# Performance work log

Measured on AMD Instinct MI355X. Metric: run time of the kernel, lower is better.

## Reference

```python
import jax, jax.numpy as jnp
import numpy as np

N, D, M, L, DEPTH, WIDTH, MPTS = 2048, 64, 2048, 16, 3, 128, 64
WIN = 2 * L + 1  # 33


def setup_inputs() -> dict:
    key = jax.random.key(0)
    ks = jax.random.split(key, 6)
    # xavier-normal-ish scales to keep sigmoids in a reasonable range
    s0 = float(np.sqrt(2.0 / (D + WIDTH)))
    s1 = float(np.sqrt(2.0 / (2 * WIDTH)))
    s2 = float(np.sqrt(2.0 / (WIDTH + WIN)))
    return {
        "u": jax.random.normal(ks[0], (MPTS, D), dtype=jnp.float32),
        "weight0": jax.random.normal(ks[1], (WIN, WIDTH, D), dtype=jnp.float32) * s0,
        "bias0": jnp.zeros((WIN, WIDTH, 1), dtype=jnp.float32),
        "weight": jax.random.normal(ks[2], (DEPTH - 1, WIN, WIDTH, WIDTH), dtype=jnp.float32) * s1,
        "bias": jnp.zeros((DEPTH - 1, WIN, WIDTH, 1), dtype=jnp.float32),
        "weight_final": jax.random.normal(ks[3], (M, WIN, WIDTH), dtype=jnp.float32) * s2,
        "bias_final": jnp.zeros((M, WIN, 1), dtype=jnp.float32),
        "xi": jax.random.normal(ks[4], (M, N + 2 * L), dtype=jnp.float32) * 0.1,
    }


def reference(u, weight0, bias0, weight, bias, weight_final, bias_final, xi):
    sig = jax.nn.sigmoid
    # first_step: shared per-frequency MLP stack
    u1 = sig(jnp.einsum('jkl,ml->jkm', weight0, u) + bias0)
    for i in range(weight.shape[0]):  # depth-1 hidden layers (small fixed count)
        u1 = sig(jnp.einsum('jkl,jlm->jkm', weight[i], u1) + bias[i])
    G = sig(jnp.einsum('ijk,jkm->ijm', weight_final, u1) + bias_final)
    # sliding-window weighted sum over spectral coeffs, vectorized as a 1D
    # cross-correlation: out[n, p] = sum_{m,j} xi[m, n+j] * G[m, j, p]
    kernel = jnp.transpose(G, (2, 0, 1))
    out = jax.lax.conv_general_dilated(
        xi[None],  # [1, M, N+2L]
        kernel,
        window_strides=(1,),
        padding='VALID',
        dimension_numbers=('NCH', 'OIH', 'NCH'),
    )  # [1, MPTS, N]
    return out[0].T  # [N, MPTS] == torch.cat over iter_prod
```

## Files before the change

kernel.cpp:

```cpp
#include <hip/hip_runtime.h>

#define WIN 33
#define WIDTH 128
#define MPTS 64
#define NN 2048
#define MM 2048
#define DD 64
#define NQ 2080

typedef __bf16 bf16x8 __attribute__((ext_vector_type(8)));
typedef float f32x4 __attribute__((ext_vector_type(4)));

__device__ __forceinline__ unsigned short f2bf(float x) {
  union { float f; unsigned int u; } v; v.f = x;
  unsigned int r = v.u + 0x7FFFu + ((v.u >> 16) & 1u);
  return (unsigned short)(r >> 16);
}
__device__ __forceinline__ float sigf(float x) { return 1.0f / (1.0f + __expf(-x)); }

__device__ __forceinline__ void gll16(const unsigned short* g, unsigned short* l) {
  __builtin_amdgcn_global_load_lds(
      (const __attribute__((address_space(1))) unsigned int*)g,
      (__attribute__((address_space(3))) unsigned int*)l, 16, 0, 0);
}

__global__ __launch_bounds__(256) void k_transpose(const float* __restrict__ xi,
                                                   unsigned short* __restrict__ xiT) {
  __shared__ float ts[64 * 37];
  int qb = blockIdx.x * 32;
  int mb = blockIdx.y * 64;
#pragma unroll
  for (int c = threadIdx.x; c < 512; c += 256) {
    int row = c >> 3, c8 = c & 7;
    float4 v = *(const float4*)&xi[(size_t)(mb + row) * NQ + qb + (c8 << 2)];
    ts[row * 37 + (c8 << 2) + 0] = v.x;
    ts[row * 37 + (c8 << 2) + 1] = v.y;
    ts[row * 37 + (c8 << 2) + 2] = v.z;
    ts[row * 37 + (c8 << 2) + 3] = v.w;
  }
  __syncthreads();
#pragma unroll
  for (int c = threadIdx.x; c < 512; c += 256) {
    int r = c >> 4, mq = c & 15;
    ushort4 h;
    h.x = f2bf(ts[(mq * 4 + 0) * 37 + r]);
    h.y = f2bf(ts[(mq * 4 + 1) * 37 + r]);
    h.z = f2bf(ts[(mq * 4 + 2) * 37 + r]);
    h.w = f2bf(ts[(mq * 4 + 3) * 37 + r]);
    *(ushort4*)&xiT[((size_t)blockIdx.y * NQ + (qb + r)) * 64 + (mq << 2)] = h;
  }
}

__global__ __launch_bounds__(256) void k_mlp(const float* __restrict__ u,
                                             const float* __restrict__ w0,
                                             const float* __restrict__ b0,
                                             const float* __restrict__ w,
                                             const float* __restrict__ bias,
                                             unsigned short* __restrict__ u1bf) {
  constexpr int WS = 72;
  constexpr int AS = 136;
  __shared__ unsigned short ws[128 * WS];
  __shared__ unsigned short actA[64 * AS];
  __shared__ unsigned short actB[64 * AS];
  __shared__ float biass[128];
  int j = blockIdx.x;
  int tid = threadIdx.x;
  int wv = tid >> 6, lane = tid & 63, l15 = lane & 15, l4 = lane >> 4;

#pragma unroll
  for (int c = tid; c < 1024; c += 256) {
    int p = c >> 4, d4 = (c & 15) << 2;
    float4 v = *(const float4*)&u[(size_t)p * DD + d4];
    ushort4 h; h.x = f2bf(v.x); h.y = f2bf(v.y); h.z = f2bf(v.z); h.w = f2bf(v.w);
    *(ushort4*)&actA[p * AS + d4] = h;
  }
#pragma unroll
  for (int c = tid; c < 2048; c += 256) {
    int k = c >> 4, d4 = (c & 15) << 2;
    float4 v = *(const float4*)&w0[((size_t)j * 128 + k) * DD + d4];
    ushort4 h; h.x = f2bf(v.x); h.y = f2bf(v.y); h.z = f2bf(v.z); h.w = f2bf(v.w);
    *(ushort4*)&ws[k * WS + d4] = h;
  }
  if (tid < 128) biass[tid] = b0[j * 128 + tid];
  __syncthreads();

  {
    f32x4 acc[2][4] = {};
#pragma unroll
    for (int t = 0; t < 2; ++t) {
      int col = (t << 5) + (l4 << 3);
      bf16x8 a[2], b[4];
#pragma unroll
      for (int s = 0; s < 2; ++s)
        a[s] = *(const bf16x8*)&ws[(wv * 32 + s * 16 + l15) * WS + col];
#pragma unroll
      for (int q = 0; q < 4; ++q)
        b[q] = *(const bf16x8*)&actA[(q * 16 + l15) * AS + col];
#pragma unroll
      for (int s = 0; s < 2; ++s)
#pragma unroll
        for (int q = 0; q < 4; ++q)
          acc[s][q] = __builtin_amdgcn_mfma_f32_16x16x32_bf16(a[s], b[q], acc[s][q], 0, 0, 0);
    }
#pragma unroll
    for (int s = 0; s < 2; ++s)
#pragma unroll
      for (int q = 0; q < 4; ++q) {
        int p = q * 16 + l15;
#pragma unroll
        for (int r = 0; r < 4; ++r) {
          int k = wv * 32 + s * 16 + (l4 << 2) + r;
          actB[p * AS + k] = f2bf(sigf(acc[s][q][r] + biass[k]));
        }
      }
  }

  unsigned short* ain = actB;
  unsigned short* aout = actA;
#pragma unroll
  for (int i = 0; i < 2; ++i) {
    f32x4 acc[2][4] = {};
    const float* wbase = w + ((size_t)i * WIN + j) * 128 * 128;
#pragma unroll
    for (int h = 0; h < 2; ++h) {
      __syncthreads();
#pragma unroll
      for (int c = tid; c < 2048; c += 256) {
        int k = c >> 4, d4 = (c & 15) << 2;
        float4 v = *(const float4*)&wbase[(size_t)k * 128 + h * 64 + d4];
        ushort4 hh; hh.x = f2bf(v.x); hh.y = f2bf(v.y); hh.z = f2bf(v.z); hh.w = f2bf(v.w);
        *(ushort4*)&ws[k * WS + d4] = hh;
      }
      if (h == 0 && tid < 128) biass[tid] = bias[((size_t)i * WIN + j) * 128 + tid];
      __syncthreads();
#pragma unroll
      for (int t = 0; t < 2; ++t) {
        int col = (t << 5) + (l4 << 3);
        bf16x8 a[2], b[4];
#pragma unroll
        for (int s = 0; s < 2; ++s)
          a[s] = *(const bf16x8*)&ws[(wv * 32 + s * 16 + l15) * WS + col];
#pragma unroll
        for (int q = 0; q < 4; ++q)
          b[q] = *(const bf16x8*)&ain[(q * 16 + l15) * AS + h * 64 + col];
#pragma unroll
        for (int s = 0; s < 2; ++s)
#pragma unroll
          for (int q = 0; q < 4; ++q)
            acc[s][q] = __builtin_amdgcn_mfma_f32_16x16x32_bf16(a[s], b[q], acc[s][q], 0, 0, 0);
      }
    }
#pragma unroll
    for (int s = 0; s < 2; ++s)
#pragma unroll
      for (int q = 0; q < 4; ++q) {
        int p = q * 16 + l15;
#pragma unroll
        for (int r = 0; r < 4; ++r) {
          int k = wv * 32 + s * 16 + (l4 << 2) + r;
          aout[p * AS + k] = f2bf(sigf(acc[s][q][r] + biass[k]));
        }
      }
    unsigned short* t2 = ain; ain = aout; aout = t2;
  }
  __syncthreads();
#pragma unroll
  for (int c = tid; c < 1024; c += 256) {
    int p = c >> 4, k8 = (c & 15) << 3;
    uint4 v = *(const uint4*)&ain[p * AS + k8];
    *(uint4*)&u1bf[((size_t)j * MPTS + p) * WIDTH + k8] = v;
  }
}

__global__ __launch_bounds__(256) void k_final(const float* __restrict__ wf,
                                               const float* __restrict__ bfin,
                                               const unsigned short* __restrict__ u1bf,
                                               unsigned short* __restrict__ Gt2) {
  constexpr int KP = 136;
  __shared__ unsigned short As[64 * KP];
  __shared__ unsigned short Bs[64 * KP];
  int bid = blockIdx.x;
  int j = bid >> 5;
  int m0 = (bid & 31) << 6;
#pragma unroll
  for (int c = threadIdx.x; c < 64 * 32; c += 256) {
    int row = c >> 5, f4 = c & 31;
    float4 v = *(const float4*)(wf + ((size_t)(m0 + row) * WIN + j) * WIDTH + (f4 << 2));
    ushort4 h;
    h.x = f2bf(v.x); h.y = f2bf(v.y); h.z = f2bf(v.z); h.w = f2bf(v.w);
    *(ushort4*)(&As[row * KP + (f4 << 2)]) = h;
  }
#pragma unroll
  for (int c = threadIdx.x; c < 64 * 16; c += 256) {
    int p = c >> 4, ch = c & 15;
    uint4 v = *(const uint4*)(u1bf + (size_t)(j * MPTS + p) * WIDTH + (ch << 3));
    *(uint4*)(&Bs[p * KP + (ch << 3)]) = v;
  }
  __syncthreads();
  int wv = threadIdx.x >> 6, lane = threadIdx.x & 63;
  int l15 = lane & 15, l4 = lane >> 4;
  f32x4 acc[4] = {};
#pragma unroll
  for (int t = 0; t < 4; ++t) {
    int col = (t << 5) + (l4 << 3);
    bf16x8 a = *(const bf16x8*)(&As[(wv * 16 + l15) * KP + col]);
#pragma unroll
    for (int q = 0; q < 4; ++q) {
      bf16x8 bb = *(const bf16x8*)(&Bs[(q * 16 + l15) * KP + col]);
      acc[q] = __builtin_amdgcn_mfma_f32_16x16x32_bf16(a, bb, acc[q], 0, 0, 0);
    }
  }
  size_t region = (size_t)((bid & 31) << 1) + (wv >> 1);
  int g = ((wv & 1) << 1) + (l4 >> 1);
  int m8 = (l4 & 1) << 2;
  int mr = m0 + wv * 16 + (l4 << 2);
#pragma unroll
  for (int q = 0; q < 4; ++q) {
    int p = q * 16 + l15;
    float z0 = acc[q][0] + bfin[(size_t)(mr + 0) * WIN + j];
    float z1 = acc[q][1] + bfin[(size_t)(mr + 1) * WIN + j];
    float z2 = acc[q][2] + bfin[(size_t)(mr + 2) * WIN + j];
    float z3 = acc[q][3] + bfin[(size_t)(mr + 3) * WIN + j];
    ushort4 st;
    st.x = f2bf(sigf(z0)); st.y = f2bf(sigf(z1));
    st.z = f2bf(sigf(z2)); st.w = f2bf(sigf(z3));
    *(ushort4*)(&Gt2[region * 67584 + ((size_t)(j * 4 + g) * 64 + p) * 8 + m8]) = st;
  }
}

__global__ __launch_bounds__(256) void k_conv(const unsigned short* __restrict__ xiT,
                                              const unsigned short* __restrict__ Gt2,
                                              float* __restrict__ out) {
  extern __shared__ unsigned short lds[];
  unsigned short* As = lds;
  unsigned short* Bs = lds + 10240;
  int bid = blockIdx.x;
  int mp = bid & 31;
  int n0 = (bid >> 5) << 7;
  int tid = threadIdx.x;
  int wv = tid >> 6, lane = tid & 63, l15 = lane & 15, l4 = lane >> 4;

  const unsigned short* Abase = xiT + (size_t)mp * (NQ * 64) + (size_t)n0 * 64;
#pragma unroll
  for (int k = 0; k < 5; ++k) {
    int instr = wv * 5 + k;
    int s = (instr << 6) + lane;
    int row = s >> 3;
    int c = (s & 7) ^ (row & 7);
    gll16(Abase + (size_t)row * 64 + (c << 3), As + (instr << 9));
  }

  f32x4 acc[2][4] = {};
#pragma unroll
  for (int half = 0; half < 2; ++half) {
    int h4 = half << 2;
#pragma unroll
    for (int ph = 0; ph < 3; ++ph) {
      int jb = ph * 11;
      if (half | ph) __syncthreads();
      const unsigned short* Bbase =
          Gt2 + (size_t)((mp << 1) + half) * 67584 + ((size_t)jb << 11);
#pragma unroll
      for (int k = 0; k < 11; ++k) {
        int instr = wv * 11 + k;
        gll16(Bbase + (((instr << 6) + lane) << 3), Bs + (instr << 9));
      }
      __syncthreads();

      bf16x8 a[2], b[4];
#pragma unroll
      for (int s = 0; s < 2; ++s) {
        int row = wv * 32 + s * 16 + l15 + jb;
        a[s] = *(const bf16x8*)&As[row * 64 + (((h4 | l4) ^ (row & 7)) << 3)];
      }
#pragma unroll
      for (int q = 0; q < 4; ++q) {
        int slot = (l4 << 6) + (q << 4) + l15;
        b[q] = *(const bf16x8*)&Bs[slot << 3];
      }
#pragma unroll
      for (int jj = 0; jj < 11; ++jj) {
        bf16x8 an[2], bn[4];
        if (jj < 10) {
#pragma unroll
          for (int s = 0; s < 2; ++s) {
            int row = wv * 32 + s * 16 + l15 + jb + jj + 1;
            an[s] = *(const bf16x8*)&As[row * 64 + (((h4 | l4) ^ (row & 7)) << 3)];
          }
#pragma unroll
          for (int q = 0; q < 4; ++q) {
            int slot = ((((jj + 1) << 2) + l4) << 6) + (q << 4) + l15;
            bn[q] = *(const bf16x8*)&Bs[slot << 3];
          }
        }
#pragma unroll
        for (int s = 0; s < 2; ++s)
#pragma unroll
          for (int q = 0; q < 4; ++q)
            acc[s][q] = __builtin_amdgcn_mfma_f32_16x16x32_bf16(a[s], b[q], acc[s][q], 0, 0, 0);
#pragma unroll
        for (int s = 0; s < 2; ++s) a[s] = an[s];
#pragma unroll
        for (int q = 0; q < 4; ++q) b[q] = bn[q];
      }
    }
  }
#pragma unroll
  for (int s = 0; s < 2; ++s)
#pragma unroll
    for (int q = 0; q < 4; ++q) {
      int nr = n0 + wv * 32 + s * 16 + (l4 << 2);
      int p = q * 16 + l15;
#pragma unroll
      for (int i = 0; i < 4; ++i)
        atomicAdd(&out[(size_t)(nr + i) * MPTS + p], acc[s][q][i]);
    }
}

extern "C" void kernel_launch(void* const* d_in, const int* in_sizes, int n_in,
                              void* d_out, int out_size, void* d_ws, size_t ws_size,
                              hipStream_t stream) {
  const float* u    = (const float*)d_in[0];
  const float* w0   = (const float*)d_in[1];
  const float* b0   = (const float*)d_in[2];
  const float* w    = (const float*)d_in[3];
  const float* bias = (const float*)d_in[4];
  const float* wf   = (const float*)d_in[5];
  const float* bfin = (const float*)d_in[6];
  const float* xi   = (const float*)d_in[7];
  float* out = (float*)d_out;
  char* ws = (char*)d_ws;
  unsigned short* xiT  = (unsigned short*)(ws);
  unsigned short* Gt2  = (unsigned short*)(ws + 8519680);
  unsigned short* u1bf = (unsigned short*)(ws + 17170432);

  hipFuncSetAttribute(reinterpret_cast<const void*>(&k_conv),
                      hipFuncAttributeMaxDynamicSharedMemorySize, 65536);

  hipMemsetAsync(out, 0, (size_t)out_size * sizeof(float), stream);
  k_transpose<<<dim3(65, 32), 256, 0, stream>>>(xi, xiT);
  k_mlp<<<WIN, 256, 0, stream>>>(u, w0, b0, w, bias, u1bf);
  k_final<<<33 * 32, 256, 0, stream>>>(wf, bfin, u1bf, Gt2);
  k_conv<<<512, 256, 65536, stream>>>(xiT, Gt2, out);
}
```

Baseline: 162.0 us.

## Double-buffer G tiles in conv kernel and stage final bias in LDS

The conv kernel's single B buffer, loaded in three 11-tap phases per half, is replaced by two LDS buffers holding 7-tap chunks. The next chunk is prefetched with global_load_lds while the current one feeds the MFMAs, hiding load latency and removing one of the two barriers per phase. LDS use rises from 64 KB to 76 KB per block, which may reduce occupancy. Separately, k_final now loads its 64 bias values into shared memory once instead of doing strided global reads in the epilogue.

```diff
diff --git a/kernel.cpp b/kernel.cpp
--- a/kernel.cpp
+++ b/kernel.cpp
@@ -179,6 +179,7 @@
   constexpr int KP = 136;
   __shared__ unsigned short As[64 * KP];
   __shared__ unsigned short Bs[64 * KP];
+  __shared__ float bfs[64];
   int bid = blockIdx.x;
   int j = bid >> 5;
   int m0 = (bid & 31) << 6;
@@ -196,6 +197,7 @@
     uint4 v = *(const uint4*)(u1bf + (size_t)(j * MPTS + p) * WIDTH + (ch << 3));
     *(uint4*)(&Bs[p * KP + (ch << 3)]) = v;
   }
+  if (threadIdx.x < 64) bfs[threadIdx.x] = bfin[(size_t)(m0 + threadIdx.x) * WIN + j];
   __syncthreads();
   int wv = threadIdx.x >> 6, lane = threadIdx.x & 63;
   int l15 = lane & 15, l4 = lane >> 4;
@@ -213,14 +215,14 @@
   size_t region = (size_t)((bid & 31) << 1) + (wv >> 1);
   int g = ((wv & 1) << 1) + (l4 >> 1);
   int m8 = (l4 & 1) << 2;
-  int mr = m0 + wv * 16 + (l4 << 2);
+  int mb = wv * 16 + (l4 << 2);
 #pragma unroll
   for (int q = 0; q < 4; ++q) {
     int p = q * 16 + l15;
-    float z0 = acc[q][0] + bfin[(size_t)(mr + 0) * WIN + j];
-    float z1 = acc[q][1] + bfin[(size_t)(mr + 1) * WIN + j];
-    float z2 = acc[q][2] + bfin[(size_t)(mr + 2) * WIN + j];
-    float z3 = acc[q][3] + bfin[(size_t)(mr + 3) * WIN + j];
+    float z0 = acc[q][0] + bfs[mb + 0];
+    float z1 = acc[q][1] + bfs[mb + 1];
+    float z2 = acc[q][2] + bfs[mb + 2];
+    float z3 = acc[q][3] + bfs[mb + 3];
     ushort4 st;
     st.x = f2bf(sigf(z0)); st.y = f2bf(sigf(z1));
     st.z = f2bf(sigf(z2)); st.w = f2bf(sigf(z3));
@@ -233,7 +235,6 @@
                                               float* __restrict__ out) {
   extern __shared__ unsigned short lds[];
   unsigned short* As = lds;
-  unsigned short* Bs = lds + 10240;
   int bid = blockIdx.x;
   int mp = bid & 31;
   int n0 = (bid >> 5) << 7;
@@ -250,23 +251,40 @@
     gll16(Abase + (size_t)row * 64 + (c << 3), As + (instr << 9));
   }
 
+  constexpr int JBT[10]  = {0, 7, 14, 21, 28, 0, 7, 14, 21, 28};
+  constexpr int CNTT[10] = {7, 7, 7, 7, 5, 7, 7, 7, 7, 5};
+  constexpr int HFT[10]  = {0, 0, 0, 0, 0, 1, 1, 1, 1, 1};
+
+  const unsigned short* Rb0 = Gt2 + (size_t)(mp << 1) * 67584;
+  const unsigned short* Rb1 = Gt2 + (size_t)((mp << 1) + 1) * 67584;
+
+  {
+    const unsigned short* Bb = Rb0;
+#pragma unroll
+    for (int k = 0; k < 7; ++k) {
+      int instr = wv * 7 + k;
+      gll16(Bb + (((instr << 6) + lane) << 3), lds + 10240 + (instr << 9));
+    }
+  }
+
   f32x4 acc[2][4] = {};
 #pragma unroll
-  for (int half = 0; half < 2; ++half) {
-    int h4 = half << 2;
-#pragma unroll
-    for (int ph = 0; ph < 3; ++ph) {
-      int jb = ph * 11;
-      if (half | ph) __syncthreads();
-      const unsigned short* Bbase =
-          Gt2 + (size_t)((mp << 1) + half) * 67584 + ((size_t)jb << 11);
-#pragma unroll
-      for (int k = 0; k < 11; ++k) {
-        int instr = wv * 11 + k;
-        gll16(Bbase + (((instr << 6) + lane) << 3), Bs + (instr << 9));
-      }
-      __syncthreads();
-
+  for (int t = 0; t < 10; ++t) {
+    __syncthreads();
+    if (t < 9) {
+      const int jbn = JBT[t + 1], cntn = CNTT[t + 1];
+      const unsigned short* Bb =
+          (HFT[t + 1] ? Rb1 : Rb0) + ((size_t)jbn << 11);
+      unsigned short* Bst = lds + 10240 + ((t + 1) & 1) * 14336;
+#pragma unroll
+      for (int k = 0; k < cntn; ++k) {
+        int instr = wv * cntn + k;
+        gll16(Bb + (((instr << 6) + lane) << 3), Bst + (instr << 9));
+      }
+    }
+    {
+      const int jb = JBT[t], cnt = CNTT[t], h4 = HFT[t] << 2;
+      const unsigned short* Bs = lds + 10240 + (t & 1) * 14336;
       bf16x8 a[2], b[4];
 #pragma unroll
       for (int s = 0; s < 2; ++s) {
@@ -279,9 +297,9 @@
         b[q] = *(const bf16x8*)&Bs[slot << 3];
       }
 #pragma unroll
-      for (int jj = 0; jj < 11; ++jj) {
+      for (int jj = 0; jj < cnt; ++jj) {
         bf16x8 an[2], bn[4];
-        if (jj < 10) {
+        if (jj < cnt - 1) {
 #pragma unroll
           for (int s = 0; s < 2; ++s) {
             int row = wv * 32 + s * 16 + l15 + jb + jj + 1;
@@ -335,11 +353,11 @@
   unsigned short* u1bf = (unsigned short*)(ws + 17170432);
 
   hipFuncSetAttribute(reinterpret_cast<const void*>(&k_conv),
-                      hipFuncAttributeMaxDynamicSharedMemorySize, 65536);
+                      hipFuncAttributeMaxDynamicSharedMemorySize, 77824);
 
   hipMemsetAsync(out, 0, (size_t)out_size * sizeof(float), stream);
   k_transpose<<<dim3(65, 32), 256, 0, stream>>>(xi, xiT);
   k_mlp<<<WIN, 256, 0, stream>>>(u, w0, b0, w, bias, u1bf);
   k_final<<<33 * 32, 256, 0, stream>>>(wf, bfin, u1bf, Gt2);
-  k_conv<<<512, 256, 65536, stream>>>(xiT, Gt2, out);
-}
+  k_conv<<<512, 256, 77824, stream>>>(xiT, Gt2, out);
+}
```

New measurement: 161.5 us. Within noise of the previous version (-0.4%).
